# Optimization experiments

Measured on AMD Instinct MI355X. Metric: run time of the kernel, lower is better.

Reference implementation:

```python
import jax, jax.numpy as jnp
import numpy as np

B, N, Z_DIM, H_DIM, MSG, MC = 32768, 16, 64, 128, 32, 4
HM_DIM = MSG * (1 + MC)          # 160
MLP_IN = MSG * MSG + HM_DIM      # 1184
MLP_HID = MSG * MSG              # 1024
MLP_OUT = MSG * MSG + MSG        # 1056


def _lin(k, fi, fo):
    return (jax.random.normal(k, (fi, fo), jnp.float32) / np.sqrt(fi)).astype(jnp.float32)


def setup_inputs() -> dict:
    key = jax.random.key(0)
    ks = jax.random.split(key, 16)
    return {
        "Z0": jax.random.normal(ks[0], (B, N, Z_DIM), jnp.float32),
        "h0": jax.random.normal(ks[1], (B, H_DIM), jnp.float32),
        "m_Z": jax.random.normal(ks[2], (B, N, MSG * MC), jnp.float32),
        "m_h": jax.random.normal(ks[3], (B, MSG * MC), jnp.float32),
        "W_Z1": _lin(ks[4], Z_DIM, MSG),                 # fc_Z1 (no bias)
        "W_h1": _lin(ks[5], H_DIM, MSG),                 # fc_h1
        "b_h1": jnp.zeros((MSG,), jnp.float32),
        "W_g1a": _lin(ks[6], HM_DIM, MSG),               # fc_g1[0]
        "b_g1a": jnp.zeros((MSG,), jnp.float32),
        "W_g1b": _lin(ks[7], MSG, 1),                    # fc_g1[2]
        "b_g1b": jnp.zeros((1,), jnp.float32),
        "W_Z2": _lin(ks[8], HM_DIM + 1, MSG),            # fc_Z2 (no bias)
        "W1": _lin(ks[9], MLP_IN, MLP_HID),              # BaseMLP
        "b1": jnp.zeros((MLP_HID,), jnp.float32),
        "W2": _lin(ks[10], MLP_HID, MLP_HID),
        "b2": jnp.zeros((MLP_HID,), jnp.float32),
        "W3": _lin(ks[11], MLP_HID, MLP_OUT),
        "b3": jnp.zeros((MLP_OUT,), jnp.float32),
    }


def reference(Z0, h0, m_Z, m_h, W_Z1, W_h1, b_h1, W_g1a, b_g1a, W_g1b, b_g1b,
              W_Z2, W1, b1, W2, b2, W3, b3):
    b = Z0.shape[0]
    Z = Z0 @ W_Z1                                        # [B,N,MSG]
    h = h0 @ W_h1 + b_h1                                 # [B,MSG]
    hm = jax.nn.relu(jnp.concatenate([h, m_h], axis=-1)) # [B,HM_DIM]
    gate = jax.nn.relu(hm @ W_g1a + b_g1a) @ W_g1b + b_g1b  # [B,1]
    # g = zeros_like(Z0)[...,0]; g[...,2]=1; g = g * fc_g1(hm)
    onehot2 = (jnp.arange(Z0.shape[1]) == 2).astype(Z0.dtype)  # [N]
    g = onehot2[None, :] * gate                          # [B,N]
    Zm = jnp.concatenate([Z, m_Z, g[..., None]], axis=-1) @ W_Z2  # [B,N,MSG]
    M = jnp.einsum('bni,bnj->bij', Zm, Zm).reshape(b, -1)  # [B,MSG*MSG]
    F_norm = jnp.linalg.norm(M, axis=-1, keepdims=True) + 1.0
    Mcat = jnp.concatenate([M, hm], axis=-1)             # [B,MLP_IN]
    Mout = jax.nn.relu(Mcat @ W1 + b1)
    Mout = jax.nn.relu(Mout @ W2 + b2)
    Mout = Mout @ W3 + b3                                # [B,MLP_OUT]
    Mout = Mout / F_norm
    msg = Zm.shape[-1]
    M_Zflat = Mout[..., : msg * msg].reshape(b, msg, msg)
    M_h = Mout[..., msg * msg:]                          # [B,MSG]
    M_Z = jnp.einsum('bnj,bjk->bnk', Zm, M_Zflat)        # [B,N,MSG]
    return (M_Z, M_h)
```

## Files before the change

kernel.cpp:

```cpp
#include <hip/hip_runtime.h>
#include <stdint.h>

#define N_B    32768
#define MLPOUT 1056
#define MCAT_K 1216
#define NPAD3  1280

typedef __attribute__((ext_vector_type(8)))  __bf16 bf16x8;
typedef __attribute__((ext_vector_type(4)))  float  f32x4;
typedef __attribute__((ext_vector_type(16))) float  f32x16;

__device__ __forceinline__ uint16_t f2bf(float f){
  union { float f; uint32_t u; } v; v.f = f;
  return (uint16_t)((v.u + 0x7fffu + ((v.u >> 16) & 1u)) >> 16);
}
__device__ __forceinline__ float bf2f(uint16_t h){
  union { uint32_t u; float f; } v; v.u = ((uint32_t)h) << 16; return v.f;
}
__device__ __forceinline__ void gld_lds16(const void* gp, void* lp){
  __builtin_amdgcn_global_load_lds(
    (__attribute__((address_space(1))) void*)(void*)gp,
    (__attribute__((address_space(3))) void*)lp, 16, 0, 0);
}

__global__ void transpose_cast_kernel(const float* __restrict__ in, uint16_t* __restrict__ out,
                                      int K, int N, int Kpad, int Npad)
{
  __shared__ float tile[32][33];
  const int tx = threadIdx.x & 31, ty = threadIdx.x >> 5;
  const int k0 = blockIdx.x * 32, n0 = blockIdx.y * 32;
#pragma unroll
  for (int i = 0; i < 4; i++){
    int k = k0 + ty + i*8, nn = n0 + tx;
    float v = (k < K && nn < N) ? in[(size_t)k*N + nn] : 0.0f;
    tile[ty + i*8][tx] = v;
  }
  __syncthreads();
#pragma unroll
  for (int i = 0; i < 4; i++){
    int nn = n0 + ty + i*8, k = k0 + tx;
    if (nn < Npad && k < Kpad) out[(size_t)nn*Kpad + k] = f2bf(tile[tx][ty + i*8]);
  }
}

__global__ void prep_small_kernel(const float* __restrict__ W_Z1, const float* __restrict__ W_Z2,
                                  const float* __restrict__ b3,
                                  uint16_t* __restrict__ WfH, uint16_t* __restrict__ WfL,
                                  float* __restrict__ wgG, float* __restrict__ b3p)
{
  __shared__ float wl[192*32];
  const int tid = threadIdx.x;
  for (int idx = tid; idx < 6144; idx += 256){
    int r = idx >> 5, c = idx & 31;
    float v;
    if (r < 64){
      v = 0.f;
      for (int i = 0; i < 32; i++) v += W_Z1[r*32 + i] * W_Z2[i*32 + c];
    } else v = W_Z2[(r - 32)*32 + c];
    wl[idx] = v;
  }
  __syncthreads();
  for (int q = tid; q < 768; q += 256){
    int lane = q & 63, ctkk = q >> 6;
    int ct = ctkk & 1, kk = ctkk >> 1;
    int c  = ct*16 + (lane & 15);
    int k0 = kk*32 + ((lane >> 4) << 3);
    for (int j = 0; j < 8; j++){
      float v = wl[(k0 + j)*32 + c];
      uint16_t hb = f2bf(v);
      WfH[q*8 + j] = hb;
      WfL[q*8 + j] = f2bf(v - bf2f(hb));
    }
  }
  if (tid < 32) wgG[tid] = W_Z2[160*32 + tid];
  for (int idx = tid; idx < NPAD3; idx += 256)
    b3p[idx] = (idx < MLPOUT) ? b3[idx] : 0.0f;
}

__global__ __launch_bounds__(256)
void gate_kernel(const float* __restrict__ h0, const float* __restrict__ mh,
                 const float* __restrict__ W_h1, const float* __restrict__ b_h1,
                 const float* __restrict__ W_g1a, const float* __restrict__ b_g1a,
                 const float* __restrict__ W_g1b, const float* __restrict__ b_g1b,
                 uint16_t* __restrict__ Mcat, float* __restrict__ gateOut)
{
  __shared__ float wh[128*32];
  __shared__ float wg[160*32];
  __shared__ float wgb[32], bh[32], bga[32];
  __shared__ float bgb;
  __shared__ float hrow[4][128];
  __shared__ float hms[4][160];
  const int tid = threadIdx.x, w = tid >> 6, l = tid & 63;
  for (int i = tid; i < 4096; i += 256) wh[i] = W_h1[i];
  for (int i = tid; i < 5120; i += 256) wg[i] = W_g1a[i];
  if (tid < 32){ wgb[tid] = W_g1b[tid]; bh[tid] = b_h1[tid]; bga[tid] = b_g1a[tid]; }
  if (tid == 0) bgb = b_g1b[0];
  __syncthreads();
  const int cg = l & 31, kh = l >> 5;
  for (int bi = 0; bi < 16; bi++){
    const int b = blockIdx.x*64 + w*16 + bi;
    hrow[w][l]      = h0[(size_t)b*128 + l];
    hrow[w][64 + l] = h0[(size_t)b*128 + 64 + l];
    float mh0 = mh[(size_t)b*128 + l];
    float mh1 = mh[(size_t)b*128 + 64 + l];
    float hacc = 0.f;
#pragma unroll 16
    for (int i = 0; i < 64; i++){
      int k = kh*64 + i;
      hacc += hrow[w][k] * wh[k*32 + cg];
    }
    hacc += __shfl_xor(hacc, 32);
    float hmc = fmaxf(hacc + bh[cg], 0.f);
    float r0 = fmaxf(mh0, 0.f), r1 = fmaxf(mh1, 0.f);
    if (l < 32) hms[w][l] = hmc;
    hms[w][32 + l] = r0;
    hms[w][96 + l] = r1;
    uint16_t* mc = Mcat + (size_t)b*MCAT_K + 1024;
    if (l < 32) mc[l] = f2bf(hmc);
    mc[32 + l] = f2bf(r0);
    mc[96 + l] = f2bf(r1);
    if (l < 32) mc[160 + l] = 0;
    float tacc = 0.f;
#pragma unroll 16
    for (int i = 0; i < 80; i++){
      int k = kh*80 + i;
      tacc += hms[w][k] * wg[k*32 + cg];
    }
    tacc += __shfl_xor(tacc, 32);
    float tc = fmaxf(tacc + bga[cg], 0.f);
    float gp = (l < 32) ? tc * wgb[cg] : 0.f;
#pragma unroll
    for (int s = 1; s < 64; s <<= 1) gp += __shfl_xor(gp, s);
    if (l == 0) gateOut[b] = gp + bgb;
  }
}

__global__ __launch_bounds__(256)
void zm_gram_kernel(const float* __restrict__ Z0, const float* __restrict__ mZ,
                    const uint16_t* __restrict__ WfH, const uint16_t* __restrict__ WfL,
                    const float* __restrict__ wgG, const float* __restrict__ gateB,
                    uint16_t* __restrict__ Mcat, float* __restrict__ Fn,
                    float* __restrict__ ZmOut)
{
  __shared__ __align__(16) uint16_t wfh[6144], wfl[6144];
  __shared__ float wgs[32];
  __shared__ __align__(16) uint16_t zhS[4][32*24], zlS[4][32*24];
  const int tid = threadIdx.x, w = tid >> 6, l = tid & 63;
#pragma unroll
  for (int i = 0; i < 3; i++){
    gld_lds16(WfH + (i*256 + tid)*8, &wfh[(i*256 + w*64)*8]);
    gld_lds16(WfL + (i*256 + tid)*8, &wfl[(i*256 + w*64)*8]);
  }
  if (tid < 32) wgs[tid] = wgG[tid];
  __syncthreads();
  const int n = l & 15, sl = l >> 4;
  for (int bi = 0; bi < 4; bi++){
    const int b = (blockIdx.x << 4) + (w << 2) + bi;
    bf16x8 xh[6], xl[6];
    const float* zp = Z0 + (size_t)b*1024 + n*64  + sl*8;
    const float* mp = mZ + (size_t)b*2048 + n*128 + sl*8;
#pragma unroll
    for (int kk = 0; kk < 6; kk++){
      const float* src = (kk < 2) ? (zp + kk*32) : (mp + (kk - 2)*32);
      float x[8];
      *(float4*)&x[0] = *(const float4*)src;
      *(float4*)&x[4] = *(const float4*)(src + 4);
#pragma unroll
      for (int j = 0; j < 8; j++){
        __bf16 h = (__bf16)x[j];
        xh[kk][j] = h;
        xl[kk][j] = (__bf16)(x[j] - (float)h);
      }
    }
    f32x4 za[2];
    za[0] = (f32x4)(0.f); za[1] = (f32x4)(0.f);
#pragma unroll
    for (int kk = 0; kk < 6; kk++){
#pragma unroll
      for (int ct = 0; ct < 2; ct++){
        bf16x8 whf = *(const bf16x8*)&wfh[((kk*2 + ct)*64 + l)*8];
        bf16x8 wlf = *(const bf16x8*)&wfl[((kk*2 + ct)*64 + l)*8];
        za[ct] = __builtin_amdgcn_mfma_f32_16x16x32_bf16(xh[kk], whf, za[ct], 0, 0, 0);
        za[ct] = __builtin_amdgcn_mfma_f32_16x16x32_bf16(xl[kk], whf, za[ct], 0, 0, 0);
        za[ct] = __builtin_amdgcn_mfma_f32_16x16x32_bf16(xh[kk], wlf, za[ct], 0, 0, 0);
      }
    }
    const float g = gateB[b];
    if (sl == 0){
      za[0][2] += g * wgs[n];
      za[1][2] += g * wgs[16 + n];
    }
    float* zo = ZmOut + (size_t)b*512;
#pragma unroll
    for (int ct = 0; ct < 2; ct++){
      ushort4 ph, pl;
#pragma unroll
      for (int r = 0; r < 4; r++){
        float v = za[ct][r];
        zo[(sl*4 + r)*32 + ct*16 + n] = v;
        uint16_t hb = f2bf(v);
        ((uint16_t*)&ph)[r] = hb;
        ((uint16_t*)&pl)[r] = f2bf(v - bf2f(hb));
      }
      const int c = ct*16 + n;
      *(ushort4*)&zhS[w][c*24 + sl*4] = ph;
      *(ushort4*)&zlS[w][c*24 + sl*4] = pl;
    }
    const int c2 = l & 31, n0 = (l >> 5) << 3;
    bf16x8 zhf = *(const bf16x8*)&zhS[w][c2*24 + n0];
    bf16x8 zlf = *(const bf16x8*)&zlS[w][c2*24 + n0];
    f32x16 gacc = (f32x16)(0.f);
    gacc = __builtin_amdgcn_mfma_f32_32x32x16_bf16(zhf, zhf, gacc, 0, 0, 0);
    gacc = __builtin_amdgcn_mfma_f32_32x32x16_bf16(zlf, zhf, gacc, 0, 0, 0);
    gacc = __builtin_amdgcn_mfma_f32_32x32x16_bf16(zhf, zlf, gacc, 0, 0, 0);
    float fs = 0.f;
#pragma unroll
    for (int i = 0; i < 16; i++) fs += gacc[i]*gacc[i];
#pragma unroll
    for (int s = 1; s < 64; s <<= 1) fs += __shfl_xor(fs, s);
    if (l == 0) Fn[b] = sqrtf(fs) + 1.0f;
    uint16_t* mcb = Mcat + (size_t)b*MCAT_K;
#pragma unroll
    for (int r = 0; r < 16; r++){
      int row = (r & 3) + 8*(r >> 2) + 4*(l >> 5);
      mcb[row*32 + c2] = f2bf(gacc[r]);
    }
  }
}

template<int NT, int RELU, int MODE, int NTN>
__global__ __launch_bounds__(512, 1)
void gemm8p_kernel(const uint16_t* __restrict__ A, const uint16_t* __restrict__ Bt,
                   const float* __restrict__ bias, uint16_t* __restrict__ outB,
                   float* __restrict__ outF, const float* __restrict__ Fn)
{
  constexpr int KK   = NT * 64;
  constexpr int NWG8 = (128 * NTN) / 8;
  __shared__ __align__(16) uint16_t lds[65536];
  const int tid = threadIdx.x;
  const int w = tid >> 6, l = tid & 63;
  const int wr = w >> 2, wc = w & 3;
  const int rA = l & 15, kq = l >> 4, swz = rA & 7;
  const int wr64 = wr * 64, wc32 = wc * 32;
  const int cs0 = ((kq)     ^ swz) * 8;
  const int cs1 = ((4 + kq) ^ swz) * 8;
  const int bid = blockIdx.x;
  const int tl  = (bid & 7) * NWG8 + (bid >> 3);
  const int m0  = (tl / NTN) * 256, n0 = (tl % NTN) * 256;

  f32x4 acc[8][4];
#pragma unroll
  for (int f = 0; f < 8; f++)
#pragma unroll
    for (int g = 0; g < 4; g++) acc[f][g] = (f32x4)(0.0f);
  uint4 aF[4][2], bF0[2][2], bF1[2][2];

#define STAGE_A(bf_, hf_, kt_) do{ \
  _Pragma("unroll") for (int j_ = 0; j_ < 2; j_++){ \
    int sl_ = j_*512 + tid; int r_ = sl_ >> 3; int c_ = (sl_ & 7) ^ (r_ & 7); \
    int rg_ = ((r_ >> 6) << 7) + (hf_)*64 + (r_ & 63); \
    gld_lds16(A + (size_t)(m0 + rg_)*KK + (kt_)*64 + c_*8, \
              &lds[(bf_)*32768 + (hf_)*8192 + (j_*512 + w*64)*8]); } }while(0)
#define STAGE_B(bf_, hf_, kt_) do{ \
  _Pragma("unroll") for (int j_ = 0; j_ < 2; j_++){ \
    int sl_ = j_*512 + tid; int r_ = sl_ >> 3; int c_ = (sl_ & 7) ^ (r_ & 7); \
    int rg_ = ((r_ >> 5) << 6) + (hf_)*32 + (r_ & 31); \
    gld_lds16(Bt + (size_t)(n0 + rg_)*KK + (kt_)*64 + c_*8, \
              &lds[(bf_)*32768 + 16384 + (hf_)*8192 + (j_*512 + w*64)*8]); } }while(0)
#define RD_A(bf_, hf_) do{ _Pragma("unroll") for (int ff_ = 0; ff_ < 4; ff_++){ \
    int ro_ = (bf_)*32768 + (hf_)*8192 + (wr64 + ff_*16 + rA)*64; \
    aF[ff_][0] = *(const uint4*)&lds[ro_ + cs0]; \
    aF[ff_][1] = *(const uint4*)&lds[ro_ + cs1]; } }while(0)
#define RD_B(dst_, bf_, hf_) do{ _Pragma("unroll") for (int gg_ = 0; gg_ < 2; gg_++){ \
    int ro_ = (bf_)*32768 + 16384 + (hf_)*8192 + (wc32 + gg_*16 + rA)*64; \
    dst_[gg_][0] = *(const uint4*)&lds[ro_ + cs0]; \
    dst_[gg_][1] = *(const uint4*)&lds[ro_ + cs1]; } }while(0)
#define MFMA16(ms_, ns_, B_) do{ _Pragma("unroll") for (int ff_ = 0; ff_ < 4; ff_++) \
  _Pragma("unroll") for (int gg_ = 0; gg_ < 2; gg_++){ \
    acc[(ms_)*4+ff_][(ns_)*2+gg_] = __builtin_amdgcn_mfma_f32_16x16x32_bf16( \
      __builtin_bit_cast(bf16x8, aF[ff_][0]), __builtin_bit_cast(bf16x8, B_[gg_][0]), \
      acc[(ms_)*4+ff_][(ns_)*2+gg_], 0, 0, 0); \
    acc[(ms_)*4+ff_][(ns_)*2+gg_] = __builtin_amdgcn_mfma_f32_16x16x32_bf16( \
      __builtin_bit_cast(bf16x8, aF[ff_][1]), __builtin_bit_cast(bf16x8, B_[gg_][1]), \
      acc[(ms_)*4+ff_][(ns_)*2+gg_], 0, 0, 0); } }while(0)
#define BAR()   asm volatile("s_barrier" ::: "memory")
#define LGKM0() asm volatile("s_waitcnt lgkmcnt(0)" ::: "memory")
#define PRIO1() __builtin_amdgcn_s_setprio(1)
#define PRIO0() __builtin_amdgcn_s_setprio(0)

  STAGE_A(0, 0, 0); STAGE_B(0, 0, 0); STAGE_A(0, 1, 0); STAGE_B(0, 1, 0);
  STAGE_A(1, 0, 1); STAGE_B(1, 0, 1); STAGE_A(1, 1, 1);
  asm volatile("s_waitcnt vmcnt(6)" ::: "memory");
  BAR();

#define ITER(BUF_, t_) do{ \
    RD_A(BUF_, 0); RD_B(bF0, BUF_, 0); \
    if ((t_) + 1 < NT) STAGE_B(1 - (BUF_), 1, (t_) + 1); \
    BAR(); LGKM0(); \
    PRIO1(); MFMA16(0, 0, bF0); PRIO0(); \
    BAR(); \
    RD_B(bF1, BUF_, 1); \
    if ((t_) + 2 < NT) STAGE_A(BUF_, 0, (t_) + 2); \
    BAR(); LGKM0(); \
    PRIO1(); MFMA16(0, 1, bF1); PRIO0(); \
    BAR(); \
    RD_A(BUF_, 1); \
    if ((t_) + 2 < NT) STAGE_B(BUF_, 0, (t_) + 2); \
    BAR(); LGKM0(); \
    PRIO1(); MFMA16(1, 0, bF0); PRIO0(); \
    BAR(); \
    if ((t_) + 2 < NT) STAGE_A(BUF_, 1, (t_) + 2); \
    BAR(); \
    PRIO1(); MFMA16(1, 1, bF1); PRIO0(); \
    if ((t_) < NT - 2)       { asm volatile("s_waitcnt vmcnt(6)" ::: "memory"); } \
    else if ((t_) == NT - 2) { asm volatile("s_waitcnt vmcnt(0)" ::: "memory"); } \
    BAR(); \
  }while(0)

#pragma unroll 1
  for (int t = 0; t + 1 < NT; t += 2){
    ITER(0, t);
    ITER(1, t + 1);
  }
  if (NT & 1) ITER(0, NT - 1);

#undef ITER
#undef STAGE_A
#undef STAGE_B
#undef RD_A
#undef RD_B
#undef MFMA16
#undef BAR
#undef LGKM0
#undef PRIO1
#undef PRIO0

#pragma unroll
  for (int f = 0; f < 8; f++){
    int grow0 = m0 + wr*128 + f*16 + kq*4;
#pragma unroll
    for (int g = 0; g < 4; g++){
      int gcol = n0 + wc*64 + g*16 + rA;
      float bv = bias[gcol];
#pragma unroll
      for (int i = 0; i < 4; i++){
        float v = acc[f][g][i] + bv;
        if (RELU) v = fmaxf(v, 0.0f);
        int grow = grow0 + i;
        if (MODE == 0){
          outB[(size_t)grow*1024 + gcol] = f2bf(v);
        } else {
          if (gcol < 1024)      outB[(size_t)grow*1024 + gcol] = f2bf(v);
          else if (gcol < 1056) outF[(size_t)grow*32 + (gcol - 1024)] = v / Fn[grow];
        }
      }
    }
  }
}

__global__ __launch_bounds__(256)
void epilogue_kernel(const uint16_t* __restrict__ Mzf, const float* __restrict__ Fn,
                     float* __restrict__ Out)
{
  __shared__ __align__(16) uint16_t mzS[4][1024];
  __shared__ __align__(16) float    zmS[4][16*36];
  const int tid = threadIdx.x, w = tid >> 6, l = tid & 63;
  const int n = l & 15, q = l >> 4;
  for (int bi = 0; bi < 4; bi++){
    const int b = (blockIdx.x << 4) + (w << 2) + bi;
    const uint4* src = (const uint4*)(Mzf + (size_t)b*1024);
    uint4* dst = (uint4*)&mzS[w][0];
    dst[l]      = src[l];
    dst[l + 64] = src[l + 64];
    const float4* zsrc = (const float4*)(Out + (size_t)b*512);
#pragma unroll
    for (int i = 0; i < 2; i++){
      int f = i*64 + l;
      int nn = f >> 3, c4 = f & 7;
      *(float4*)&zmS[w][nn*36 + c4*4] = zsrc[f];
    }
    float acc[8];
#pragma unroll
    for (int i = 0; i < 8; i++) acc[i] = 0.f;
#pragma unroll
    for (int j = 0; j < 32; j++){
      float zv = zmS[w][n*36 + j];
      uint4 mv = *(const uint4*)&mzS[w][j*32 + q*8];
      acc[0] += zv * bf2f((uint16_t)(mv.x & 0xffffu));
      acc[1] += zv * bf2f((uint16_t)(mv.x >> 16));
      acc[2] += zv * bf2f((uint16_t)(mv.y & 0xffffu));
      acc[3] += zv * bf2f((uint16_t)(mv.y >> 16));
      acc[4] += zv * bf2f((uint16_t)(mv.z & 0xffffu));
      acc[5] += zv * bf2f((uint16_t)(mv.z >> 16));
      acc[6] += zv * bf2f((uint16_t)(mv.w & 0xffffu));
      acc[7] += zv * bf2f((uint16_t)(mv.w >> 16));
    }
    const float inv = 1.0f / Fn[b];
    float4* op = (float4*)(Out + (size_t)b*512 + n*32 + q*8);
    op[0] = make_float4(acc[0]*inv, acc[1]*inv, acc[2]*inv, acc[3]*inv);
    op[1] = make_float4(acc[4]*inv, acc[5]*inv, acc[6]*inv, acc[7]*inv);
  }
}

extern "C" void kernel_launch(void* const* d_in, const int* in_sizes, int n_in,
                              void* d_out, int out_size, void* d_ws, size_t ws_size,
                              hipStream_t stream)
{
  const float* Z0    = (const float*)d_in[0];
  const float* h0    = (const float*)d_in[1];
  const float* mZ    = (const float*)d_in[2];
  const float* mh    = (const float*)d_in[3];
  const float* W_Z1  = (const float*)d_in[4];
  const float* W_h1  = (const float*)d_in[5];
  const float* b_h1  = (const float*)d_in[6];
  const float* W_g1a = (const float*)d_in[7];
  const float* b_g1a = (const float*)d_in[8];
  const float* W_g1b = (const float*)d_in[9];
  const float* b_g1b = (const float*)d_in[10];
  const float* W_Z2  = (const float*)d_in[11];
  const float* W1    = (const float*)d_in[12];
  const float* b1    = (const float*)d_in[13];
  const float* W2    = (const float*)d_in[14];
  const float* b2    = (const float*)d_in[15];
  const float* W3    = (const float*)d_in[16];
  const float* b3    = (const float*)d_in[17];

  char* ws = (char*)d_ws;
  size_t off = 0;
  auto alloc = [&](size_t bytes) -> char* {
    char* p = ws + off;
    off += (bytes + 255) & ~(size_t)255;
    return p;
  };
  uint16_t* W1t  = (uint16_t*)alloc((size_t)1024*MCAT_K*2);
  uint16_t* W2t  = (uint16_t*)alloc((size_t)1024*1024*2);
  uint16_t* W3t  = (uint16_t*)alloc((size_t)NPAD3*1024*2);
  float*    b3p  = (float*)   alloc((size_t)NPAD3*4);
  uint16_t* WfH  = (uint16_t*)alloc((size_t)6144*2);
  uint16_t* WfL  = (uint16_t*)alloc((size_t)6144*2);
  float*    wgG  = (float*)   alloc((size_t)32*4);
  float*    gate = (float*)   alloc((size_t)N_B*4);
  float*    Fn   = (float*)   alloc((size_t)N_B*4);
  uint16_t* Mcat = (uint16_t*)alloc((size_t)N_B*MCAT_K*2);
  uint16_t* H1   = (uint16_t*)alloc((size_t)N_B*1024*2);
  uint16_t* H2   = (uint16_t*)alloc((size_t)N_B*1024*2);
  uint16_t* Mzf  = Mcat;
  float* OutMZ = (float*)d_out;
  float* OutMH = (float*)d_out + (size_t)N_B*512;

  transpose_cast_kernel<<<dim3(38,32), 256, 0, stream>>>(W1, W1t, 1184, 1024, MCAT_K, 1024);
  transpose_cast_kernel<<<dim3(32,32), 256, 0, stream>>>(W2, W2t, 1024, 1024, 1024, 1024);
  transpose_cast_kernel<<<dim3(32,40), 256, 0, stream>>>(W3, W3t, 1024, 1056, 1024, NPAD3);
  prep_small_kernel<<<1, 256, 0, stream>>>(W_Z1, W_Z2, b3, WfH, WfL, wgG, b3p);
  gate_kernel<<<512, 256, 0, stream>>>(h0, mh, W_h1, b_h1, W_g1a, b_g1a, W_g1b, b_g1b,
                                       Mcat, gate);
  zm_gram_kernel<<<2048, 256, 0, stream>>>(Z0, mZ, WfH, WfL, wgG, gate, Mcat, Fn, OutMZ);
  gemm8p_kernel<19,1,0,4><<<512, 512, 0, stream>>>(Mcat, W1t, b1, H1, nullptr, nullptr);
  gemm8p_kernel<16,1,0,4><<<512, 512, 0, stream>>>(H1,   W2t, b2, H2, nullptr, nullptr);
  gemm8p_kernel<16,0,1,5><<<640, 512, 0, stream>>>(H2,   W3t, b3p, Mzf, OutMH, Fn);
  epilogue_kernel<<<2048, 256, 0, stream>>>(Mzf, Fn, OutMZ);
}
```

Before: 557.8 us.

## Replace fine-grained 8-wave ping-pong GEMM schedule with simple double-buffered loop

Replaces the interleaved schedule in the MLP GEMM main loop, which used many barriers, lgkmcnt waits, setprio and partial vmcnt waits to stage half-tiles two steps ahead. Each iteration now issues all global-to-LDS loads for the next tile up front, reads the current tile's fragments and runs all MFMAs. It then waits for every outstanding load before one barrier. This cuts barrier and priority overhead and leaves LDS-read ordering to the compiler, at the cost of only one tile of prefetch depth and a full vmcnt(0) drain every iteration.

```diff
diff --git a/kernel.cpp b/kernel.cpp
--- a/kernel.cpp
+++ b/kernel.cpp
@@ -284,56 +284,39 @@
       __builtin_bit_cast(bf16x8, aF[ff_][1]), __builtin_bit_cast(bf16x8, B_[gg_][1]), \
       acc[(ms_)*4+ff_][(ns_)*2+gg_], 0, 0, 0); } }while(0)
 #define BAR()   asm volatile("s_barrier" ::: "memory")
-#define LGKM0() asm volatile("s_waitcnt lgkmcnt(0)" ::: "memory")
-#define PRIO1() __builtin_amdgcn_s_setprio(1)
-#define PRIO0() __builtin_amdgcn_s_setprio(0)
-
-  STAGE_A(0, 0, 0); STAGE_B(0, 0, 0); STAGE_A(0, 1, 0); STAGE_B(0, 1, 0);
-  STAGE_A(1, 0, 1); STAGE_B(1, 0, 1); STAGE_A(1, 1, 1);
-  asm volatile("s_waitcnt vmcnt(6)" ::: "memory");
+
+  STAGE_A(0, 0, 0); STAGE_A(0, 1, 0); STAGE_B(0, 0, 0); STAGE_B(0, 1, 0);
+  asm volatile("s_waitcnt vmcnt(0)" ::: "memory");
   BAR();
 
-#define ITER(BUF_, t_) do{ \
-    RD_A(BUF_, 0); RD_B(bF0, BUF_, 0); \
-    if ((t_) + 1 < NT) STAGE_B(1 - (BUF_), 1, (t_) + 1); \
-    BAR(); LGKM0(); \
-    PRIO1(); MFMA16(0, 0, bF0); PRIO0(); \
-    BAR(); \
-    RD_B(bF1, BUF_, 1); \
-    if ((t_) + 2 < NT) STAGE_A(BUF_, 0, (t_) + 2); \
-    BAR(); LGKM0(); \
-    PRIO1(); MFMA16(0, 1, bF1); PRIO0(); \
-    BAR(); \
+#define ITER2(BUF_, t_) do{ \
+    if ((t_) + 1 < NT){ \
+      STAGE_A(1 - (BUF_), 0, (t_) + 1); STAGE_A(1 - (BUF_), 1, (t_) + 1); \
+      STAGE_B(1 - (BUF_), 0, (t_) + 1); STAGE_B(1 - (BUF_), 1, (t_) + 1); \
+    } \
+    RD_B(bF0, BUF_, 0); RD_B(bF1, BUF_, 1); \
+    RD_A(BUF_, 0); \
+    MFMA16(0, 0, bF0); MFMA16(0, 1, bF1); \
     RD_A(BUF_, 1); \
-    if ((t_) + 2 < NT) STAGE_B(BUF_, 0, (t_) + 2); \
-    BAR(); LGKM0(); \
-    PRIO1(); MFMA16(1, 0, bF0); PRIO0(); \
-    BAR(); \
-    if ((t_) + 2 < NT) STAGE_A(BUF_, 1, (t_) + 2); \
-    BAR(); \
-    PRIO1(); MFMA16(1, 1, bF1); PRIO0(); \
-    if ((t_) < NT - 2)       { asm volatile("s_waitcnt vmcnt(6)" ::: "memory"); } \
-    else if ((t_) == NT - 2) { asm volatile("s_waitcnt vmcnt(0)" ::: "memory"); } \
+    MFMA16(1, 0, bF0); MFMA16(1, 1, bF1); \
+    if ((t_) + 1 < NT){ asm volatile("s_waitcnt vmcnt(0)" ::: "memory"); } \
     BAR(); \
   }while(0)
 
 #pragma unroll 1
   for (int t = 0; t + 1 < NT; t += 2){
-    ITER(0, t);
-    ITER(1, t + 1);
-  }
-  if (NT & 1) ITER(0, NT - 1);
-
-#undef ITER
+    ITER2(0, t);
+    ITER2(1, t + 1);
+  }
+  if (NT & 1) ITER2(0, NT - 1);
+
+#undef ITER2
 #undef STAGE_A
 #undef STAGE_B
 #undef RD_A
 #undef RD_B
 #undef MFMA16
 #undef BAR
-#undef LGKM0
-#undef PRIO1
-#undef PRIO0
 
 #pragma unroll
   for (int f = 0; f < 8; f++){
```

Result: faster. 542.3 us (-2.8%).
